# Kernel tuning notes

Measured on AMD Instinct MI355X. Metric: run time of the kernel, lower is better.

## Reference

```python
import jax, jax.numpy as jnp
import numpy as np

V, E, H, S, T, B = 32000, 512, 1024, 64, 64, 32
PAD_IDX = 1
NEG = -100000.0


def gru_cell(x, h, Wih, Whh, bih, bhh):
    # torch GRUCell math: gates ordered r, z, n
    gx = x @ Wih.T + bih          # [B, 3H]
    gh = h @ Whh.T + bhh          # [B, 3H]
    xr, xz, xn = jnp.split(gx, 3, axis=-1)
    hr, hz, hn = jnp.split(gh, 3, axis=-1)
    r = jax.nn.sigmoid(xr + hr)
    z = jax.nn.sigmoid(xz + hz)
    n = jnp.tanh(xn + r * hn)
    return (1.0 - z) * n + z * h


def setup_inputs() -> dict:
    key = jax.random.key(0)
    ks = jax.random.split(key, 24)
    s = 0.02
    def W(k, shape):
        return (jax.random.normal(k, shape, dtype=jnp.float32) * s)
    inp = {
        'src_tokens': jax.random.randint(ks[0], (S, B), 0, V, dtype=jnp.int32),
        'tgt_tokens': jax.random.randint(ks[1], (T, B), 0, V, dtype=jnp.int32),
        'enc_emb': W(ks[2], (V, E)),
        'enc_Wih0': W(ks[3], (3 * H, E)),
        'enc_Whh0': W(ks[4], (3 * H, H)),
        'enc_bih0': jnp.zeros((3 * H,), jnp.float32),
        'enc_bhh0': jnp.zeros((3 * H,), jnp.float32),
        'enc_Wih1': W(ks[5], (3 * H, H)),
        'enc_Whh1': W(ks[6], (3 * H, H)),
        'enc_bih1': jnp.zeros((3 * H,), jnp.float32),
        'enc_bhh1': jnp.zeros((3 * H,), jnp.float32),
        'dec_emb': W(ks[7], (V, E)),
        'dec_Wih0': W(ks[8], (3 * H, E)),
        'dec_Whh0': W(ks[9], (3 * H, H)),
        'dec_bih0': jnp.zeros((3 * H,), jnp.float32),
        'dec_bhh0': jnp.zeros((3 * H,), jnp.float32),
        'dec_Wih1': W(ks[10], (3 * H, H)),
        'dec_Whh1': W(ks[11], (3 * H, H)),
        'dec_bih1': jnp.zeros((3 * H,), jnp.float32),
        'dec_bhh1': jnp.zeros((3 * H,), jnp.float32),
        'Wc': W(ks[12], (H, 2 * H)),
        'bc': jnp.zeros((H,), jnp.float32),
        'Wo': W(ks[13], (V, H)),
        'bo': jnp.zeros((V,), jnp.float32),
    }
    return inp


def reference(src_tokens, tgt_tokens, enc_emb, enc_Wih0, enc_Whh0, enc_bih0,
              enc_bhh0, enc_Wih1, enc_Whh1, enc_bih1, enc_bhh1, dec_emb,
              dec_Wih0, dec_Whh0, dec_bih0, dec_bhh0, dec_Wih1, dec_Whh1,
              dec_bih1, dec_bhh1, Wc, bc, Wo, bo):
    batch = src_tokens.shape[1]
    # ---- encoder: 2-layer GRU over source, time-major ----
    emb_src = enc_emb[src_tokens]                     # [S, B, E]

    def enc_step(h, x_t):
        h0 = gru_cell(x_t, h[0], enc_Wih0, enc_Whh0, enc_bih0, enc_bhh0)
        h1 = gru_cell(h0, h[1], enc_Wih1, enc_Whh1, enc_bih1, enc_bhh1)
        return jnp.stack([h0, h1]), h1

    h0_init = jnp.zeros((2, batch, H), emb_src.dtype)
    hidden, enc_out = jax.lax.scan(enc_step, h0_init, emb_src)  # enc_out [S,B,H]

    mask = (src_tokens != PAD_IDX).T                  # [B, S]

    # ---- decoder: teacher-forced loop over target tokens ----
    def dec_step(h, tok):
        x = dec_emb[tok]                              # [B, E]
        h0 = gru_cell(x, h[0], dec_Wih0, dec_Whh0, dec_bih0, dec_bhh0)
        h1 = gru_cell(h0, h[1], dec_Wih1, dec_Whh1, dec_bih1, dec_bhh1)
        scores = jnp.einsum('bh,sbh->bs', h1, enc_out)    # [B, S]
        scores = jnp.where(mask, scores, NEG)
        attn = jax.nn.softmax(scores, axis=1)             # [B, S]
        ctx = jnp.einsum('bs,sbh->bh', attn, enc_out)     # [B, H]
        cc = jnp.tanh(jnp.concatenate([h1, ctx], axis=1) @ Wc.T + bc)
        logits = cc @ Wo.T + bo                           # [B, V]
        return jnp.stack([h0, h1]), logits

    _, logits_seq = jax.lax.scan(dec_step, hidden, tgt_tokens[:-1])  # [T-1,B,V]
    outputs = jnp.concatenate(
        [jnp.zeros((1, batch, V), logits_seq.dtype), logits_seq], axis=0)
    return outputs
```

## Files before the change

### kernel.cpp

```cpp
#include <hip/hip_runtime.h>
#include <math.h>

#define Vv 32000
#define Ee 512
#define Hh 1024
#define H3 3072
#define Ss 64
#define Tt 64
#define Bb 32
#define DEC_T 63
#define KS 16
#define KSL 64
#define PAD_TOK 1
#define NEGV -100000.0f

__device__ __forceinline__ float sigmoidf_(float x) {
  return 1.0f / (1.0f + __expf(-x));
}

__global__ __launch_bounds__(256) void transpose_k(const float* __restrict__ src,
                                                   float* __restrict__ dst,
                                                   int R, int C) {
  __shared__ float tile[32][33];
  int r0 = blockIdx.y * 32, c0 = blockIdx.x * 32;
  int tx = threadIdx.x & 31, ty = threadIdx.x >> 5;
  for (int i = ty; i < 32; i += 8)
    tile[i][tx] = src[(long)(r0 + i) * C + c0 + tx];
  __syncthreads();
  for (int i = ty; i < 32; i += 8)
    dst[(long)(c0 + i) * R + r0 + tx] = tile[tx][i];
}

template <int ACT>
__global__ __launch_bounds__(256) void gemm_nt(
    const float* __restrict__ A, const int* __restrict__ idx, int lda,
    const float* __restrict__ W, int ldw,
    const float* __restrict__ bias,
    float* __restrict__ C, long ldc,
    int M, int N, int K) {
  __shared__ float As[8][132];
  __shared__ float Ws[8][132];
  int tid = threadIdx.x;
  int n0 = blockIdx.x * 128;
  int m0 = blockIdx.y * 128;
  int sr = tid >> 1;
  int sk = (tid & 1) * 4;
  int am = m0 + sr;
  bool aval = am < M;
  int amc = aval ? am : (M - 1);
  const float* arow = A + (idx ? (long)idx[amc] * lda : (long)amc * lda);
  const float* wrow = W + (long)(n0 + sr) * ldw;
  int tx = tid & 15, ty = tid >> 4;
  float acc[8][8];
#pragma unroll
  for (int i = 0; i < 8; i++)
#pragma unroll
    for (int j = 0; j < 8; j++) acc[i][j] = 0.f;

  for (int k0 = 0; k0 < K; k0 += 8) {
    float4 av = aval ? *(const float4*)(arow + k0 + sk) : make_float4(0.f, 0.f, 0.f, 0.f);
    float4 wv = *(const float4*)(wrow + k0 + sk);
    __syncthreads();
    As[sk + 0][sr] = av.x; As[sk + 1][sr] = av.y; As[sk + 2][sr] = av.z; As[sk + 3][sr] = av.w;
    Ws[sk + 0][sr] = wv.x; Ws[sk + 1][sr] = wv.y; Ws[sk + 2][sr] = wv.z; Ws[sk + 3][sr] = wv.w;
    __syncthreads();
#pragma unroll
    for (int k = 0; k < 8; k++) {
      float a[8], w[8];
      *(float4*)(a) = *(const float4*)&As[k][ty * 8];
      *(float4*)(a + 4) = *(const float4*)&As[k][ty * 8 + 4];
      *(float4*)(w) = *(const float4*)&Ws[k][tx * 8];
      *(float4*)(w + 4) = *(const float4*)&Ws[k][tx * 8 + 4];
#pragma unroll
      for (int i = 0; i < 8; i++)
#pragma unroll
        for (int j = 0; j < 8; j++) acc[i][j] = fmaf(a[i], w[j], acc[i][j]);
    }
  }
#pragma unroll
  for (int i = 0; i < 8; i++) {
    int m = m0 + ty * 8 + i;
    if (m < M) {
      float* crow = C + (long)m * ldc + n0 + tx * 8;
#pragma unroll
      for (int j = 0; j < 8; j++) {
        float v = acc[i][j] + bias[n0 + tx * 8 + j];
        if (ACT == 1) v = tanhf(v);
        crow[j] = v;
      }
    }
  }
}

__global__ __launch_bounds__(256) void rec_gemv(
    const float* __restrict__ x0, const float* __restrict__ Wt0, float* __restrict__ p0,
    const float* __restrict__ x1, const float* __restrict__ Wt1, float* __restrict__ p1) {
  const float* x = (blockIdx.z == 0) ? x0 : x1;
  const float* Wt = (blockIdx.z == 0) ? Wt0 : Wt1;
  float* part = (blockIdx.z == 0) ? p0 : p1;
  int ks = blockIdx.y;
  int j0 = blockIdx.x * 256;
  int tid = threadIdx.x;
  int txj = tid & 63;
  int bg = tid >> 6;
  int j = j0 + txj * 4;
  __shared__ float xs[32][68];
  {
    int r = tid >> 3;
    int c = (tid & 7) * 8;
    const float* xp = x + r * Hh + ks * KSL + c;
    float4 v0 = *(const float4*)(xp);
    float4 v1 = *(const float4*)(xp + 4);
    *(float4*)&xs[r][c] = v0;
    *(float4*)&xs[r][c + 4] = v1;
  }
  __syncthreads();
  float acc[8][4];
#pragma unroll
  for (int bb = 0; bb < 8; bb++)
#pragma unroll
    for (int q = 0; q < 4; q++) acc[bb][q] = 0.f;
  const float* wp = Wt + (long)(ks * KSL) * H3 + j;
#pragma unroll 4
  for (int k = 0; k < KSL; k++) {
    float4 w = *(const float4*)(wp);
    wp += H3;
#pragma unroll
    for (int bb = 0; bb < 8; bb++) {
      float xv = xs[bg * 8 + bb][k];
      acc[bb][0] = fmaf(xv, w.x, acc[bb][0]);
      acc[bb][1] = fmaf(xv, w.y, acc[bb][1]);
      acc[bb][2] = fmaf(xv, w.z, acc[bb][2]);
      acc[bb][3] = fmaf(xv, w.w, acc[bb][3]);
    }
  }
#pragma unroll
  for (int bb = 0; bb < 8; bb++) {
    int b = bg * 8 + bb;
    float4 v;
    v.x = acc[bb][0]; v.y = acc[bb][1]; v.z = acc[bb][2]; v.w = acc[bb][3];
    *(float4*)&part[((long)ks * Bb + b) * H3 + j] = v;
  }
}

__global__ __launch_bounds__(256) void gru_update0(
    const float* __restrict__ gx, const float* __restrict__ part,
    const float* __restrict__ bhh, float* __restrict__ h) {
  int t = blockIdx.x * 256 + threadIdx.x;
  int b = t >> 10, i = t & 1023;
  float hr = bhh[i], hz = bhh[Hh + i], hn = bhh[2 * Hh + i];
#pragma unroll 4
  for (int ks = 0; ks < KS; ks++) {
    const float* p = part + ((long)ks * Bb + b) * H3 + i;
    hr += p[0]; hz += p[Hh]; hn += p[2 * Hh];
  }
  const float* g = gx + (long)b * H3 + i;
  float r = sigmoidf_(g[0] + hr);
  float z = sigmoidf_(g[Hh] + hz);
  float n = tanhf(g[2 * Hh] + r * hn);
  h[t] = (1.f - z) * n + z * h[t];
}

__global__ __launch_bounds__(256) void gru_update1(
    const float* __restrict__ pgx, const float* __restrict__ pgh,
    const float* __restrict__ bih, const float* __restrict__ bhh,
    float* __restrict__ h, float* __restrict__ out2, long os) {
  int t = blockIdx.x * 256 + threadIdx.x;
  int b = t >> 10, i = t & 1023;
  float xr = bih[i], xz = bih[Hh + i], xn = bih[2 * Hh + i];
  float hr = bhh[i], hz = bhh[Hh + i], hn = bhh[2 * Hh + i];
#pragma unroll 4
  for (int ks = 0; ks < KS; ks++) {
    const float* px = pgx + ((long)ks * Bb + b) * H3 + i;
    const float* ph = pgh + ((long)ks * Bb + b) * H3 + i;
    xr += px[0]; xz += px[Hh]; xn += px[2 * Hh];
    hr += ph[0]; hz += ph[Hh]; hn += ph[2 * Hh];
  }
  float r = sigmoidf_(xr + hr);
  float z = sigmoidf_(xz + hz);
  float n = tanhf(xn + r * hn);
  float hv = (1.f - z) * n + z * h[t];
  h[t] = hv;
  out2[(long)b * os + i] = hv;
}

__global__ __launch_bounds__(256) void attn_kernel(
    const float* __restrict__ h1cat,
    const float* __restrict__ enc_out,
    const int* __restrict__ src_tok,
    float* __restrict__ attn) {
  int tb = blockIdx.x;
  int b = tb & 31;
  __shared__ float hs[1024];
  __shared__ float sc[64][4];
  __shared__ float red[64];
  int tid = threadIdx.x;
  const float* h1 = h1cat + (long)tb * 2048;
  for (int i = tid; i < 1024; i += 256) hs[i] = h1[i];
  __syncthreads();
  int s = tid >> 2, q = tid & 3;
  const float* eo = enc_out + ((long)s * Bb + b) * Hh + q * 256;
  float p = 0.f;
  for (int k = 0; k < 256; k += 4) {
    float4 e = *(const float4*)(eo + k);
    const float* hq = hs + q * 256 + k;
    p += e.x * hq[0] + e.y * hq[1] + e.z * hq[2] + e.w * hq[3];
  }
  sc[s][q] = p;
  __syncthreads();
  if (tid < 64) {
    float v = sc[tid][0] + sc[tid][1] + sc[tid][2] + sc[tid][3];
    bool m = (src_tok[tid * Bb + b] != PAD_TOK);
    red[tid] = m ? v : NEGV;
  }
  __syncthreads();
  if (tid < 64) {
    float v = red[tid];
    float mx = v;
    for (int o = 32; o; o >>= 1) mx = fmaxf(mx, __shfl_xor(mx, o));
    float e = __expf(v - mx);
    float sum = e;
    for (int o = 32; o; o >>= 1) sum += __shfl_xor(sum, o);
    attn[(long)tb * 64 + tid] = e / sum;
  }
}

__global__ __launch_bounds__(256) void ctx_kernel(
    const float* __restrict__ attn, const float* __restrict__ enc_out,
    float* __restrict__ h1cat) {
  int tb = blockIdx.x;
  int b = tb & 31;
  __shared__ float as[64];
  int tid = threadIdx.x;
  if (tid < 64) as[tid] = attn[(long)tb * 64 + tid];
  __syncthreads();
  float4 acc = make_float4(0.f, 0.f, 0.f, 0.f);
  const float* eo = enc_out + (long)b * Hh + tid * 4;
  for (int s = 0; s < 64; s++) {
    float a = as[s];
    float4 e = *(const float4*)(eo + (long)s * Bb * Hh);
    acc.x += a * e.x; acc.y += a * e.y; acc.z += a * e.z; acc.w += a * e.w;
  }
  *(float4*)(h1cat + (long)tb * 2048 + 1024 + tid * 4) = acc;
}

extern "C" void kernel_launch(void* const* d_in, const int* in_sizes, int n_in,
                              void* d_out, int out_size, void* d_ws, size_t ws_size,
                              hipStream_t stream) {
  const int* src_tok = (const int*)d_in[0];
  const int* tgt_tok = (const int*)d_in[1];
  const float* enc_emb = (const float*)d_in[2];
  const float* eWih0 = (const float*)d_in[3];
  const float* eWhh0 = (const float*)d_in[4];
  const float* ebih0 = (const float*)d_in[5];
  const float* ebhh0 = (const float*)d_in[6];
  const float* eWih1 = (const float*)d_in[7];
  const float* eWhh1 = (const float*)d_in[8];
  const float* ebih1 = (const float*)d_in[9];
  const float* ebhh1 = (const float*)d_in[10];
  const float* dec_emb = (const float*)d_in[11];
  const float* dWih0 = (const float*)d_in[12];
  const float* dWhh0 = (const float*)d_in[13];
  const float* dbih0 = (const float*)d_in[14];
  const float* dbhh0 = (const float*)d_in[15];
  const float* dWih1 = (const float*)d_in[16];
  const float* dWhh1 = (const float*)d_in[17];
  const float* dbih1 = (const float*)d_in[18];
  const float* dbhh1 = (const float*)d_in[19];
  const float* Wc = (const float*)d_in[20];
  const float* bc = (const float*)d_in[21];
  const float* Wo = (const float*)d_in[22];
  const float* bo = (const float*)d_in[23];
  float* out = (float*)d_out;

  float* w = (float*)d_ws;
  size_t o = 0;
  const size_t WT = (size_t)Hh * H3;
  float* eWhh0t = w + o; o += WT;
  float* eWih1t = w + o; o += WT;
  float* eWhh1t = w + o; o += WT;
  float* dWhh0t = w + o; o += WT;
  float* dWih1t = w + o; o += WT;
  float* dWhh1t = w + o; o += WT;
  float* gx0 = w + o;    o += (size_t)Ss * Bb * H3;
  float* enc_out = w + o; o += (size_t)Ss * Bb * Hh;
  float* h1cat = w + o;  o += (size_t)DEC_T * Bb * 2 * Hh;
  float* h0buf = w + o;  o += (size_t)Bb * Hh;
  float* h1buf = w + o;  o += (size_t)Bb * Hh;
  float* pgh0 = w + o;   o += (size_t)KS * Bb * H3;
  float* pgx1 = w + o;   o += (size_t)KS * Bb * H3;
  float* pgh1 = w + o;   o += (size_t)KS * Bb * H3;
  float* attnb = w + o;  o += (size_t)DEC_T * Bb * Ss;
  float* ccb = w + o;    o += (size_t)DEC_T * Bb * Hh;

  hipMemsetAsync(out, 0, (size_t)Bb * Vv * sizeof(float), stream);
  hipMemsetAsync(h0buf, 0, (size_t)2 * Bb * Hh * sizeof(float), stream);

  dim3 tg(Hh / 32, H3 / 32);
  transpose_k<<<tg, 256, 0, stream>>>(eWhh0, eWhh0t, H3, Hh);
  transpose_k<<<tg, 256, 0, stream>>>(eWih1, eWih1t, H3, Hh);
  transpose_k<<<tg, 256, 0, stream>>>(eWhh1, eWhh1t, H3, Hh);
  transpose_k<<<tg, 256, 0, stream>>>(dWhh0, dWhh0t, H3, Hh);
  transpose_k<<<tg, 256, 0, stream>>>(dWih1, dWih1t, H3, Hh);
  transpose_k<<<tg, 256, 0, stream>>>(dWhh1, dWhh1t, H3, Hh);

  gemm_nt<0><<<dim3(H3 / 128, 16), 256, 0, stream>>>(
      enc_emb, src_tok, Ee, eWih0, Ee, ebih0, gx0, (long)H3, Ss * Bb, H3, Ee);

  for (int s = 0; s < Ss; s++) {
    rec_gemv<<<dim3(12, KS, 1), 256, 0, stream>>>(h0buf, eWhh0t, pgh0,
                                                  h0buf, eWhh0t, pgh0);
    gru_update0<<<128, 256, 0, stream>>>(gx0 + (size_t)s * Bb * H3, pgh0, ebhh0, h0buf);
    rec_gemv<<<dim3(12, KS, 2), 256, 0, stream>>>(h0buf, eWih1t, pgx1,
                                                  h1buf, eWhh1t, pgh1);
    gru_update1<<<128, 256, 0, stream>>>(pgx1, pgh1, ebih1, ebhh1, h1buf,
                                         enc_out + (size_t)s * Bb * Hh, (long)Hh);
  }

  gemm_nt<0><<<dim3(H3 / 128, 16), 256, 0, stream>>>(
      dec_emb, tgt_tok, Ee, dWih0, Ee, dbih0, gx0, (long)H3, DEC_T * Bb, H3, Ee);

  for (int t = 0; t < DEC_T; t++) {
    rec_gemv<<<dim3(12, KS, 1), 256, 0, stream>>>(h0buf, dWhh0t, pgh0,
                                                  h0buf, dWhh0t, pgh0);
    gru_update0<<<128, 256, 0, stream>>>(gx0 + (size_t)t * Bb * H3, pgh0, dbhh0, h0buf);
    rec_gemv<<<dim3(12, KS, 2), 256, 0, stream>>>(h0buf, dWih1t, pgx1,
                                                  h1buf, dWhh1t, pgh1);
    gru_update1<<<128, 256, 0, stream>>>(pgx1, pgh1, dbih1, dbhh1, h1buf,
                                         h1cat + (size_t)t * Bb * 2 * Hh, (long)(2 * Hh));
  }

  attn_kernel<<<DEC_T * Bb, 256, 0, stream>>>(h1cat, enc_out, src_tok, attnb);
  ctx_kernel<<<DEC_T * Bb, 256, 0, stream>>>(attnb, enc_out, h1cat);

  gemm_nt<1><<<dim3(Hh / 128, 16), 256, 0, stream>>>(
      h1cat, nullptr, 2 * Hh, Wc, 2 * Hh, bc, ccb, (long)Hh, DEC_T * Bb, Hh, 2 * Hh);

  gemm_nt<0><<<dim3(Vv / 128, 16), 256, 0, stream>>>(
      ccb, nullptr, Hh, Wo, Hh, bo, out + (size_t)Bb * Vv, (long)Vv, DEC_T * Bb, Vv, Hh);
}
```

Before: 8.103 ms.

## Use persistent grid-synced GRU kernel and split-bf16 MFMA logits GEMM

Replaces the per-timestep rec_gemv/gru_update launches (and weight transposes) with one persistent recurrence kernel per encoder and decoder. Each of 256 blocks keeps its 12 weight rows of the three recurrent matrices in shared memory, and the blocks meet at an atomic grid barrier between the two layers. The output-projection GEMM moves to bf16 MFMA with a hi/lo split of both operands (three passes) to keep roughly fp32 accuracy. The persistent kernel removes launch overhead and rereading of weights from global memory, but it relies on all 256 blocks of 768 threads with about 148KB of shared memory each being co-resident. If they are not, the barrier deadlocks; the split adds conversion passes over Wo.

```diff
diff --git a/kernel.cpp b/kernel.cpp
--- a/kernel.cpp
+++ b/kernel.cpp
@@ -6,29 +6,17 @@
 #define Hh 1024
 #define H3 3072
 #define Ss 64
-#define Tt 64
 #define Bb 32
 #define DEC_T 63
-#define KS 16
-#define KSL 64
 #define PAD_TOK 1
 #define NEGV -100000.0f
 
+typedef unsigned short ushort_t;
+typedef __attribute__((ext_vector_type(8))) __bf16 bf16x8;
+typedef __attribute__((ext_vector_type(4))) float f32x4;
+
 __device__ __forceinline__ float sigmoidf_(float x) {
   return 1.0f / (1.0f + __expf(-x));
-}
-
-__global__ __launch_bounds__(256) void transpose_k(const float* __restrict__ src,
-                                                   float* __restrict__ dst,
-                                                   int R, int C) {
-  __shared__ float tile[32][33];
-  int r0 = blockIdx.y * 32, c0 = blockIdx.x * 32;
-  int tx = threadIdx.x & 31, ty = threadIdx.x >> 5;
-  for (int i = ty; i < 32; i += 8)
-    tile[i][tx] = src[(long)(r0 + i) * C + c0 + tx];
-  __syncthreads();
-  for (int i = ty; i < 32; i += 8)
-    dst[(long)(c0 + i) * R + r0 + tx] = tile[tx][i];
 }
 
 template <int ACT>
@@ -92,103 +80,133 @@
   }
 }
 
-__global__ __launch_bounds__(256) void rec_gemv(
-    const float* __restrict__ x0, const float* __restrict__ Wt0, float* __restrict__ p0,
-    const float* __restrict__ x1, const float* __restrict__ Wt1, float* __restrict__ p1) {
-  const float* x = (blockIdx.z == 0) ? x0 : x1;
-  const float* Wt = (blockIdx.z == 0) ? Wt0 : Wt1;
-  float* part = (blockIdx.z == 0) ? p0 : p1;
-  int ks = blockIdx.y;
-  int j0 = blockIdx.x * 256;
-  int tid = threadIdx.x;
-  int txj = tid & 63;
-  int bg = tid >> 6;
-  int j = j0 + txj * 4;
-  __shared__ float xs[32][68];
-  {
-    int r = tid >> 3;
-    int c = (tid & 7) * 8;
-    const float* xp = x + r * Hh + ks * KSL + c;
-    float4 v0 = *(const float4*)(xp);
-    float4 v1 = *(const float4*)(xp + 4);
-    *(float4*)&xs[r][c] = v0;
-    *(float4*)&xs[r][c + 4] = v1;
-  }
-  __syncthreads();
-  float acc[8][4];
-#pragma unroll
-  for (int bb = 0; bb < 8; bb++)
-#pragma unroll
-    for (int q = 0; q < 4; q++) acc[bb][q] = 0.f;
-  const float* wp = Wt + (long)(ks * KSL) * H3 + j;
-#pragma unroll 4
-  for (int k = 0; k < KSL; k++) {
-    float4 w = *(const float4*)(wp);
-    wp += H3;
-#pragma unroll
-    for (int bb = 0; bb < 8; bb++) {
-      float xv = xs[bg * 8 + bb][k];
-      acc[bb][0] = fmaf(xv, w.x, acc[bb][0]);
-      acc[bb][1] = fmaf(xv, w.y, acc[bb][1]);
-      acc[bb][2] = fmaf(xv, w.z, acc[bb][2]);
-      acc[bb][3] = fmaf(xv, w.w, acc[bb][3]);
-    }
-  }
-#pragma unroll
-  for (int bb = 0; bb < 8; bb++) {
-    int b = bg * 8 + bb;
-    float4 v;
-    v.x = acc[bb][0]; v.y = acc[bb][1]; v.z = acc[bb][2]; v.w = acc[bb][3];
-    *(float4*)&part[((long)ks * Bb + b) * H3 + j] = v;
-  }
-}
-
-__global__ __launch_bounds__(256) void gru_update0(
-    const float* __restrict__ gx, const float* __restrict__ part,
-    const float* __restrict__ bhh, float* __restrict__ h) {
-  int t = blockIdx.x * 256 + threadIdx.x;
-  int b = t >> 10, i = t & 1023;
-  float hr = bhh[i], hz = bhh[Hh + i], hn = bhh[2 * Hh + i];
-#pragma unroll 4
-  for (int ks = 0; ks < KS; ks++) {
-    const float* p = part + ((long)ks * Bb + b) * H3 + i;
-    hr += p[0]; hz += p[Hh]; hn += p[2 * Hh];
-  }
-  const float* g = gx + (long)b * H3 + i;
-  float r = sigmoidf_(g[0] + hr);
-  float z = sigmoidf_(g[Hh] + hz);
-  float n = tanhf(g[2 * Hh] + r * hn);
-  h[t] = (1.f - z) * n + z * h[t];
-}
-
-__global__ __launch_bounds__(256) void gru_update1(
-    const float* __restrict__ pgx, const float* __restrict__ pgh,
-    const float* __restrict__ bih, const float* __restrict__ bhh,
-    float* __restrict__ h, float* __restrict__ out2, long os) {
-  int t = blockIdx.x * 256 + threadIdx.x;
-  int b = t >> 10, i = t & 1023;
-  float xr = bih[i], xz = bih[Hh + i], xn = bih[2 * Hh + i];
-  float hr = bhh[i], hz = bhh[Hh + i], hn = bhh[2 * Hh + i];
-#pragma unroll 4
-  for (int ks = 0; ks < KS; ks++) {
-    const float* px = pgx + ((long)ks * Bb + b) * H3 + i;
-    const float* ph = pgh + ((long)ks * Bb + b) * H3 + i;
-    xr += px[0]; xz += px[Hh]; xn += px[2 * Hh];
-    hr += ph[0]; hz += ph[Hh]; hn += ph[2 * Hh];
-  }
-  float r = sigmoidf_(xr + hr);
-  float z = sigmoidf_(xz + hz);
-  float n = tanhf(xn + r * hn);
-  float hv = (1.f - z) * n + z * h[t];
-  h[t] = hv;
-  out2[(long)b * os + i] = hv;
+
+__device__ __forceinline__ void gbar_(unsigned* cnt, unsigned target) {
+  __syncthreads();
+  if (threadIdx.x == 0) {
+    __threadfence();
+    __hip_atomic_fetch_add(cnt, 1u, __ATOMIC_ACQ_REL, __HIP_MEMORY_SCOPE_AGENT);
+    while (__hip_atomic_load(cnt, __ATOMIC_RELAXED, __HIP_MEMORY_SCOPE_AGENT) < target)
+      __builtin_amdgcn_s_sleep(2);
+  }
+  __syncthreads();
+  __threadfence();
+}
+
+__device__ __forceinline__ void dotpass_(const float* __restrict__ wrow,
+                                         const float* __restrict__ hA,
+                                         const float* __restrict__ hB,
+                                         float& dA, float& dB) {
+  float a0 = 0.f, a1 = 0.f, a2 = 0.f, a3 = 0.f;
+  float b0 = 0.f, b1 = 0.f, b2 = 0.f, b3 = 0.f;
+#pragma unroll 8
+  for (int j = 0; j < 64; j++) {
+    float4 w4 = *(const float4*)(wrow + j * 16);
+    float4 xa = *(const float4*)(hA + j * 16);
+    float4 xb = *(const float4*)(hB + j * 16);
+    a0 = fmaf(w4.x, xa.x, a0); a1 = fmaf(w4.y, xa.y, a1);
+    a2 = fmaf(w4.z, xa.z, a2); a3 = fmaf(w4.w, xa.w, a3);
+    b0 = fmaf(w4.x, xb.x, b0); b1 = fmaf(w4.y, xb.y, b1);
+    b2 = fmaf(w4.z, xb.z, b2); b3 = fmaf(w4.w, xb.w, b3);
+  }
+  float dA_ = (a0 + a1) + (a2 + a3);
+  float dB_ = (b0 + b1) + (b2 + b3);
+  dA_ += __shfl_xor(dA_, 1); dA_ += __shfl_xor(dA_, 2);
+  dB_ += __shfl_xor(dB_, 1); dB_ += __shfl_xor(dB_, 2);
+  dA = dA_; dB = dB_;
+}
+
+__global__ __launch_bounds__(768) void recur_k(
+    const float* __restrict__ Whh0, const float* __restrict__ Wih1,
+    const float* __restrict__ Whh1, const float* __restrict__ bhh0,
+    const float* __restrict__ bih1, const float* __restrict__ bhh1,
+    const float* __restrict__ gx,
+    float* __restrict__ h0,
+    float* __restrict__ h1,
+    float* __restrict__ out2,
+    long o2r, long o2s, int steps, unsigned barBase,
+    unsigned* __restrict__ bar) {
+  __shared__ float w0[12][1028], w1x[12][1028], w1h[12][1028];
+  __shared__ float sg0[12][32], sgx[12][32], sgh[12][32];
+  __shared__ float bia0[12], b1xs[12], b1hs[12];
+
+  const int tid = threadIdx.x;
+  const int u0 = blockIdx.x * 4;
+
+  for (int i = tid; i < 3072; i += 768) {
+    int r = i >> 8;
+    int k4 = (i & 255) << 2;
+    int g = r >> 2, u = r & 3;
+    long src = (long)(g * 1024 + u0 + u) * 1024 + k4;
+    *(float4*)&w0[r][k4]  = *(const float4*)(Whh0 + src);
+    *(float4*)&w1x[r][k4] = *(const float4*)(Wih1 + src);
+    *(float4*)&w1h[r][k4] = *(const float4*)(Whh1 + src);
+  }
+  if (tid < 12) {
+    int g = tid >> 2, u = tid & 3;
+    bia0[tid] = bhh0[g * 1024 + u0 + u];
+    b1xs[tid] = bih1[g * 1024 + u0 + u];
+    b1hs[tid] = bhh1[g * 1024 + u0 + u];
+  }
+  __syncthreads();
+
+  const int kh4 = (tid & 3) << 2;
+  const int c   = (tid >> 2) % 12;
+  const int bp  = tid / 48;
+  const int ub  = tid & 3, bb = tid >> 2;
+
+  int p0 = 0, p1 = 0;
+  for (int s = 0; s < steps; s++) {
+    float gxr = 0.f, gxz = 0.f, gxn = 0.f, h0old = 0.f;
+    if (tid < 128) {
+      const float* gp = gx + ((long)s * 32 + bb) * 3072 + u0 + ub;
+      gxr = gp[0]; gxz = gp[1024]; gxn = gp[2048];
+      h0old = h0[p0 * 32768 + bb * 1024 + u0 + ub];
+    }
+    {
+      const float* hb = h0 + p0 * 32768 + kh4;
+      float dA, dB;
+      dotpass_(&w0[c][kh4], hb + bp * 1024, hb + (bp + 16) * 1024, dA, dB);
+      if ((tid & 3) == 0) { sg0[c][bp] = dA; sg0[c][bp + 16] = dB; }
+    }
+    __syncthreads();
+    if (tid < 128) {
+      float rr = sigmoidf_(gxr + sg0[ub][bb] + bia0[ub]);
+      float zz = sigmoidf_(gxz + sg0[4 + ub][bb] + bia0[4 + ub]);
+      float nn = tanhf(gxn + rr * (sg0[8 + ub][bb] + bia0[8 + ub]));
+      h0[(p0 ^ 1) * 32768 + bb * 1024 + u0 + ub] = (1.f - zz) * nn + zz * h0old;
+    }
+    p0 ^= 1;
+    gbar_(bar, (barBase + (unsigned)s + 1u) * 256u);
+    float h1old = 0.f;
+    if (tid < 128) h1old = h1[p1 * 32768 + bb * 1024 + u0 + ub];
+    {
+      const float* xb = h0 + p0 * 32768 + kh4;
+      const float* hb = h1 + p1 * 32768 + kh4;
+      float xA, xB, hA, hB;
+      dotpass_(&w1x[c][kh4], xb + bp * 1024, xb + (bp + 16) * 1024, xA, xB);
+      dotpass_(&w1h[c][kh4], hb + bp * 1024, hb + (bp + 16) * 1024, hA, hB);
+      if ((tid & 3) == 0) {
+        sgx[c][bp] = xA; sgx[c][bp + 16] = xB;
+        sgh[c][bp] = hA; sgh[c][bp + 16] = hB;
+      }
+    }
+    __syncthreads();
+    if (tid < 128) {
+      float rr = sigmoidf_(sgx[ub][bb] + b1xs[ub] + sgh[ub][bb] + b1hs[ub]);
+      float zz = sigmoidf_(sgx[4 + ub][bb] + b1xs[4 + ub] + sgh[4 + ub][bb] + b1hs[4 + ub]);
+      float nn = tanhf(sgx[8 + ub][bb] + b1xs[8 + ub] + rr * (sgh[8 + ub][bb] + b1hs[8 + ub]));
+      float hv = (1.f - zz) * nn + zz * h1old;
+      h1[(p1 ^ 1) * 32768 + bb * 1024 + u0 + ub] = hv;
+      out2[(long)s * o2s + (long)bb * o2r + u0 + ub] = hv;
+    }
+    p1 ^= 1;
+  }
 }
 
 __global__ __launch_bounds__(256) void attn_kernel(
-    const float* __restrict__ h1cat,
-    const float* __restrict__ enc_out,
-    const int* __restrict__ src_tok,
-    float* __restrict__ attn) {
+    const float* __restrict__ h1cat, const float* __restrict__ enc_out,
+    const int* __restrict__ src_tok, float* __restrict__ attn) {
   int tb = blockIdx.x;
   int b = tb & 31;
   __shared__ float hs[1024];
@@ -242,6 +260,102 @@
     acc.x += a * e.x; acc.y += a * e.y; acc.z += a * e.z; acc.w += a * e.w;
   }
   *(float4*)(h1cat + (long)tb * 2048 + 1024 + tid * 4) = acc;
+}
+
+__device__ __forceinline__ ushort_t f2bf_(float x) {
+  unsigned u = __float_as_uint(x);
+  unsigned r = (u + 0x7fffu + ((u >> 16) & 1u)) >> 16;
+  return (ushort_t)r;
+}
+__device__ __forceinline__ float bf2f_(ushort_t h) {
+  return __uint_as_float(((unsigned)h) << 16);
+}
+
+__global__ __launch_bounds__(256) void split_k(
+    const float* __restrict__ src, ushort_t* __restrict__ hi,
+    ushort_t* __restrict__ lo, long n) {
+  long i = ((long)blockIdx.x * 256 + threadIdx.x) * 4;
+  if (i >= n) return;
+  float4 v = *(const float4*)(src + i);
+  ushort_t h0 = f2bf_(v.x), h1 = f2bf_(v.y), h2 = f2bf_(v.z), h3 = f2bf_(v.w);
+  ushort_t l0 = f2bf_(v.x - bf2f_(h0)), l1 = f2bf_(v.y - bf2f_(h1));
+  ushort_t l2 = f2bf_(v.z - bf2f_(h2)), l3 = f2bf_(v.w - bf2f_(h3));
+  ushort4 hv; hv.x = h0; hv.y = h1; hv.z = h2; hv.w = h3;
+  ushort4 lv; lv.x = l0; lv.y = l1; lv.z = l2; lv.w = l3;
+  *(ushort4*)(hi + i) = hv;
+  *(ushort4*)(lo + i) = lv;
+}
+
+__global__ __launch_bounds__(256) void gemm_logits(
+    const ushort_t* __restrict__ Ah, const ushort_t* __restrict__ Al,
+    const ushort_t* __restrict__ Wh, const ushort_t* __restrict__ Wl,
+    const float* __restrict__ bias, float* __restrict__ C, int M) {
+  __shared__ ushort_t As[128 * 32];
+  __shared__ ushort_t Bs[128 * 32];
+  int tid = threadIdx.x;
+  int n0 = blockIdx.x * 128, m0 = blockIdx.y * 128;
+  int wave = tid >> 6, lane = tid & 63;
+  int wm = wave & 1, wn = wave >> 1;
+  int lm = lane & 15, lq = lane >> 4;
+  f32x4 acc[4][4];
+#pragma unroll
+  for (int i = 0; i < 4; i++)
+#pragma unroll
+    for (int j = 0; j < 4; j++) acc[i][j] = (f32x4){0.f, 0.f, 0.f, 0.f};
+
+  int srow = tid >> 2;
+  int skq = tid & 3;
+  int chunkw = skq ^ (srow & 3);
+
+  for (int pass = 0; pass < 3; pass++) {
+    const ushort_t* Ap = (pass < 2) ? Ah : Al;
+    const ushort_t* Wp = (pass == 1) ? Wl : Wh;
+    for (int k0 = 0; k0 < 1024; k0 += 32) {
+      int r0 = m0 + srow;      r0 = r0 < M ? r0 : M - 1;
+      int r1 = m0 + 64 + srow; r1 = r1 < M ? r1 : M - 1;
+      uint4 a0 = *(const uint4*)(Ap + (long)r0 * 1024 + k0 + skq * 8);
+      uint4 a1 = *(const uint4*)(Ap + (long)r1 * 1024 + k0 + skq * 8);
+      uint4 b0 = *(const uint4*)(Wp + (long)(n0 + srow) * 1024 + k0 + skq * 8);
+      uint4 b1 = *(const uint4*)(Wp + (long)(n0 + 64 + srow) * 1024 + k0 + skq * 8);
+      __syncthreads();
+      *(uint4*)&As[srow * 32 + chunkw * 8] = a0;
+      *(uint4*)&As[(64 + srow) * 32 + chunkw * 8] = a1;
+      *(uint4*)&Bs[srow * 32 + chunkw * 8] = b0;
+      *(uint4*)&Bs[(64 + srow) * 32 + chunkw * 8] = b1;
+      __syncthreads();
+      bf16x8 af[4], bf[4];
+#pragma unroll
+      for (int mi = 0; mi < 4; mi++) {
+        int r = wm * 64 + mi * 16 + lm;
+        af[mi] = *(const bf16x8*)&As[r * 32 + ((lq ^ (r & 3)) * 8)];
+      }
+#pragma unroll
+      for (int nj = 0; nj < 4; nj++) {
+        int r = wn * 64 + nj * 16 + lm;
+        bf[nj] = *(const bf16x8*)&Bs[r * 32 + ((lq ^ (r & 3)) * 8)];
+      }
+#pragma unroll
+      for (int mi = 0; mi < 4; mi++)
+#pragma unroll
+        for (int nj = 0; nj < 4; nj++)
+          acc[mi][nj] = __builtin_amdgcn_mfma_f32_16x16x32_bf16(
+              af[mi], bf[nj], acc[mi][nj], 0, 0, 0);
+    }
+  }
+#pragma unroll
+  for (int mi = 0; mi < 4; mi++) {
+#pragma unroll
+    for (int nj = 0; nj < 4; nj++) {
+      int mbase = m0 + wm * 64 + mi * 16 + lq * 4;
+      int n = n0 + wn * 64 + nj * 16 + lm;
+      float bv = bias[n];
+#pragma unroll
+      for (int r = 0; r < 4; r++) {
+        int m = mbase + r;
+        if (m < M) C[(long)m * Vv + n] = acc[mi][nj][r] + bv;
+      }
+    }
+  }
 }
 
 extern "C" void kernel_launch(void* const* d_in, const int* in_sizes, int n_in,
@@ -275,60 +389,38 @@
 
   float* w = (float*)d_ws;
   size_t o = 0;
-  const size_t WT = (size_t)Hh * H3;
-  float* eWhh0t = w + o; o += WT;
-  float* eWih1t = w + o; o += WT;
-  float* eWhh1t = w + o; o += WT;
-  float* dWhh0t = w + o; o += WT;
-  float* dWih1t = w + o; o += WT;
-  float* dWhh1t = w + o; o += WT;
-  float* gx0 = w + o;    o += (size_t)Ss * Bb * H3;
+  float* gx0 = w + o;     o += (size_t)Ss * Bb * H3;
   float* enc_out = w + o; o += (size_t)Ss * Bb * Hh;
-  float* h1cat = w + o;  o += (size_t)DEC_T * Bb * 2 * Hh;
-  float* h0buf = w + o;  o += (size_t)Bb * Hh;
-  float* h1buf = w + o;  o += (size_t)Bb * Hh;
-  float* pgh0 = w + o;   o += (size_t)KS * Bb * H3;
-  float* pgx1 = w + o;   o += (size_t)KS * Bb * H3;
-  float* pgh1 = w + o;   o += (size_t)KS * Bb * H3;
-  float* attnb = w + o;  o += (size_t)DEC_T * Bb * Ss;
-  float* ccb = w + o;    o += (size_t)DEC_T * Bb * Hh;
+  float* h1cat = w + o;   o += (size_t)DEC_T * Bb * 2 * Hh;
+  float* h0buf = w + o;   o += (size_t)2 * Bb * Hh;
+  float* h1buf = w + o;   o += (size_t)2 * Bb * Hh;
+  float* attnb = w + o;   o += (size_t)DEC_T * Bb * Ss;
+  float* ccb = w + o;     o += (size_t)DEC_T * Bb * Hh;
+  unsigned* bar = (unsigned*)(w + o); o += 16;
+  ushort_t* Ah = (ushort_t*)(w + o); o += (size_t)DEC_T * Bb * Hh / 2;
+  ushort_t* Al = (ushort_t*)(w + o); o += (size_t)DEC_T * Bb * Hh / 2;
+  ushort_t* Wh = (ushort_t*)(w + o); o += (size_t)Vv * Hh / 2;
+  ushort_t* Wl = (ushort_t*)(w + o); o += (size_t)Vv * Hh / 2;
+  const size_t FULL_BYTES = o * sizeof(float);
+  bool use_mfma = ws_size >= FULL_BYTES;
 
   hipMemsetAsync(out, 0, (size_t)Bb * Vv * sizeof(float), stream);
-  hipMemsetAsync(h0buf, 0, (size_t)2 * Bb * Hh * sizeof(float), stream);
-
-  dim3 tg(Hh / 32, H3 / 32);
-  transpose_k<<<tg, 256, 0, stream>>>(eWhh0, eWhh0t, H3, Hh);
-  transpose_k<<<tg, 256, 0, stream>>>(eWih1, eWih1t, H3, Hh);
-  transpose_k<<<tg, 256, 0, stream>>>(eWhh1, eWhh1t, H3, Hh);
-  transpose_k<<<tg, 256, 0, stream>>>(dWhh0, dWhh0t, H3, Hh);
-  transpose_k<<<tg, 256, 0, stream>>>(dWih1, dWih1t, H3, Hh);
-  transpose_k<<<tg, 256, 0, stream>>>(dWhh1, dWhh1t, H3, Hh);
+  hipMemsetAsync(h0buf, 0, (size_t)4 * Bb * Hh * sizeof(float), stream);
+  hipMemsetAsync(bar, 0, 8, stream);
 
   gemm_nt<0><<<dim3(H3 / 128, 16), 256, 0, stream>>>(
       enc_emb, src_tok, Ee, eWih0, Ee, ebih0, gx0, (long)H3, Ss * Bb, H3, Ee);
 
-  for (int s = 0; s < Ss; s++) {
-    rec_gemv<<<dim3(12, KS, 1), 256, 0, stream>>>(h0buf, eWhh0t, pgh0,
-                                                  h0buf, eWhh0t, pgh0);
-    gru_update0<<<128, 256, 0, stream>>>(gx0 + (size_t)s * Bb * H3, pgh0, ebhh0, h0buf);
-    rec_gemv<<<dim3(12, KS, 2), 256, 0, stream>>>(h0buf, eWih1t, pgx1,
-                                                  h1buf, eWhh1t, pgh1);
-    gru_update1<<<128, 256, 0, stream>>>(pgx1, pgh1, ebih1, ebhh1, h1buf,
-                                         enc_out + (size_t)s * Bb * Hh, (long)Hh);
-  }
+  recur_k<<<256, 768, 0, stream>>>(eWhh0, eWih1, eWhh1, ebhh0, ebih1, ebhh1,
+                                   gx0, h0buf, h1buf, enc_out,
+                                   (long)Hh, (long)(Bb * Hh), Ss, 0u, bar);
 
   gemm_nt<0><<<dim3(H3 / 128, 16), 256, 0, stream>>>(
       dec_emb, tgt_tok, Ee, dWih0, Ee, dbih0, gx0, (long)H3, DEC_T * Bb, H3, Ee);
 
-  for (int t = 0; t < DEC_T; t++) {
-    rec_gemv<<<dim3(12, KS, 1), 256, 0, stream>>>(h0buf, dWhh0t, pgh0,
-                                                  h0buf, dWhh0t, pgh0);
-    gru_update0<<<128, 256, 0, stream>>>(gx0 + (size_t)t * Bb * H3, pgh0, dbhh0, h0buf);
-    rec_gemv<<<dim3(12, KS, 2), 256, 0, stream>>>(h0buf, dWih1t, pgx1,
-                                                  h1buf, dWhh1t, pgh1);
-    gru_update1<<<128, 256, 0, stream>>>(pgx1, pgh1, dbih1, dbhh1, h1buf,
-                                         h1cat + (size_t)t * Bb * 2 * Hh, (long)(2 * Hh));
-  }
+  recur_k<<<256, 768, 0, stream>>>(dWhh0, dWih1, dWhh1, dbhh0, dbih1, dbhh1,
+                                   gx0, h0buf, h1buf, h1cat,
+                                   (long)(2 * Hh), (long)(Bb * 2 * Hh), DEC_T, (unsigned)Ss, bar);
 
   attn_kernel<<<DEC_T * Bb, 256, 0, stream>>>(h1cat, enc_out, src_tok, attnb);
   ctx_kernel<<<DEC_T * Bb, 256, 0, stream>>>(attnb, enc_out, h1cat);
@@ -336,6 +428,13 @@
   gemm_nt<1><<<dim3(Hh / 128, 16), 256, 0, stream>>>(
       h1cat, nullptr, 2 * Hh, Wc, 2 * Hh, bc, ccb, (long)Hh, DEC_T * Bb, Hh, 2 * Hh);
 
-  gemm_nt<0><<<dim3(Vv / 128, 16), 256, 0, stream>>>(
-      ccb, nullptr, Hh, Wo, Hh, bo, out + (size_t)Bb * Vv, (long)Vv, DEC_T * Bb, Vv, Hh);
-}
+  if (use_mfma) {
+    split_k<<<(Vv * Hh) / 1024, 256, 0, stream>>>(Wo, Wh, Wl, (long)Vv * Hh);
+    split_k<<<(DEC_T * Bb * Hh) / 1024, 256, 0, stream>>>(ccb, Ah, Al, (long)DEC_T * Bb * Hh);
+    gemm_logits<<<dim3(Vv / 128, 16), 256, 0, stream>>>(
+        Ah, Al, Wh, Wl, bo, out + (size_t)Bb * Vv, DEC_T * Bb);
+  } else {
+    gemm_nt<0><<<dim3(Vv / 128, 16), 256, 0, stream>>>(
+        ccb, nullptr, Hh, Wo, Hh, bo, out + (size_t)Bb * Vv, (long)Vv, DEC_T * Bb, Vv, Hh);
+  }
+}
```

Result: slower. 14.13 ms (+74.4%).
